# Performance work log

Measured on AMD Instinct MI355X. Metric: run time of the kernel, lower is better.

Reference implementation:

```python
import jax, jax.numpy as jnp
import numpy as np

L, D, H, DH, DF = 4, 512, 8, 64, 2048
B, S = 4, 2048
EPS = 1e-6  # fast-transformers causal-linear eps


def _ln(x, g, b, eps=1e-5):
    mu = jnp.mean(x, axis=-1, keepdims=True)
    var = jnp.var(x, axis=-1, keepdims=True)
    return (x - mu) * jax.lax.rsqrt(var + eps) * g + b


def _causal_linear(Q, K, V):
    # Q, K, V: [B, S, H, DH]; O(N) linear-attention recurrence over S
    Qs = jnp.moveaxis(Q, 1, 0)
    Ks = jnp.moveaxis(K, 1, 0)
    Vs = jnp.moveaxis(V, 1, 0)
    b = Q.shape[0]
    kv0 = jnp.zeros((b, H, DH, DH), Q.dtype)  # running sum of k v^T
    z0 = jnp.zeros((b, H, DH), Q.dtype)       # running sum of k

    def step(carry, qkv):
        kv, z = carry
        q, k, v = qkv  # each [B, H, DH]
        kv = kv + k[..., :, None] * v[..., None, :]
        z = z + k
        num = jnp.einsum('bhd,bhdm->bhm', q, kv)
        den = jnp.einsum('bhd,bhd->bh', q, z) + EPS
        return (kv, z), num / den[..., None]

    _, out = jax.lax.scan(step, (kv0, z0), (Qs, Ks, Vs))
    return jnp.moveaxis(out, 0, 1)  # [B, S, H, DH]


def _layer(x, p):
    Wq, bq, Wk, bk, Wv, bv, Wo, bo, W1, b1, W2, b2, g1, be1, g2, be2 = p
    b, s, _ = x.shape
    q = (x @ Wq + bq).reshape(b, s, H, DH)
    k = (x @ Wk + bk).reshape(b, s, H, DH)
    v = (x @ Wv + bv).reshape(b, s, H, DH)
    Qf = jax.nn.elu(q) + 1.0  # feature map phi(x) = elu(x) + 1
    Kf = jax.nn.elu(k) + 1.0
    a = _causal_linear(Qf, Kf, v).reshape(b, s, D)
    x = x + (a @ Wo + bo)            # residual (dropout=0)
    x = _ln(x, g1, be1)              # post-norm
    y = jax.nn.gelu(x @ W1 + b1, approximate=False) @ W2 + b2
    return _ln(x + y, g2, be2)


def _encoder(h, params, gf, bef):
    def body(x, p):
        return _layer(x, p), None
    x, _ = jax.lax.scan(body, h, params)
    return _ln(x, gf, bef)  # final LayerNorm from builder


def setup_inputs() -> dict:
    key = jax.random.key(0)
    ks = jax.random.split(key, 8)

    def w(k, shape, fan_in):
        return jax.random.normal(k, shape, jnp.float32) * (fan_in ** -0.5)

    return {
        'h': jax.random.normal(ks[0], (B, S, D), jnp.float32),
        'Wq': w(ks[1], (L, D, D), D), 'bq': jnp.zeros((L, D), jnp.float32),
        'Wk': w(ks[2], (L, D, D), D), 'bk': jnp.zeros((L, D), jnp.float32),
        'Wv': w(ks[3], (L, D, D), D), 'bv': jnp.zeros((L, D), jnp.float32),
        'Wo': w(ks[4], (L, D, D), D), 'bo': jnp.zeros((L, D), jnp.float32),
        'W1': w(ks[5], (L, D, DF), D), 'b1': jnp.zeros((L, DF), jnp.float32),
        'W2': w(ks[6], (L, DF, D), DF), 'b2': jnp.zeros((L, D), jnp.float32),
        'g1': jnp.ones((L, D), jnp.float32), 'be1': jnp.zeros((L, D), jnp.float32),
        'g2': jnp.ones((L, D), jnp.float32), 'be2': jnp.zeros((L, D), jnp.float32),
        'gf': jnp.ones((D,), jnp.float32), 'bef': jnp.zeros((D,), jnp.float32),
    }


def reference(h, Wq, bq, Wk, bk, Wv, bv, Wo, bo, W1, b1, W2, b2,
              g1, be1, g2, be2, gf, bef):
    params = (Wq, bq, Wk, bk, Wv, bv, Wo, bo, W1, b1, W2, b2, g1, be1, g2, be2)
    return _encoder(h, params, gf, bef)
```

## Files before the change

kernel.cpp:

```cpp
#include <hip/hip_runtime.h>
#include <hip/hip_bf16.h>
#include <math.h>

#define LAYERS 4
#define DMODEL 512
#define NH 8
#define DH 64
#define DFF 2048
#define NB 4
#define S_LEN 2048
#define MROWS 8192
#define CHUNK 64
#define NCHUNK 32
#define ATT_EPS 1e-6f
#define LN_EPS 1e-5f
#define SEGSTRIDE (MROWS * DMODEL)

typedef __attribute__((ext_vector_type(8))) short short8v;
typedef __attribute__((ext_vector_type(4))) float f32x4;

__device__ __forceinline__ float b2f(unsigned short u) {
    union { float f; unsigned u; } c; c.u = ((unsigned)u) << 16; return c.f;
}
__device__ __forceinline__ unsigned short f2b(float f) {
    union { float f; unsigned u; } c; c.f = f;
    unsigned r = c.u + 0x7FFFu + ((c.u >> 16) & 1u);
    return (unsigned short)(r >> 16);
}
__device__ __forceinline__ void gload16(const void* g, void* l) {
    __builtin_amdgcn_global_load_lds(
        (const __attribute__((address_space(1))) void*)g,
        (__attribute__((address_space(3))) void*)l, 16, 0, 0);
}
__device__ __forceinline__ float elu1f(float v) {
    return (v > 0.f) ? (v + 1.f) : __expf(v);
}
__device__ __forceinline__ float geluf(float v) {
    float u = 0.7978845608028654f * v * (1.f + 0.044715f * v * v);
    float th = 1.f - 2.f / (1.f + __expf(2.f * u));
    return 0.5f * v * (1.f + th);
}

template <int ACT, bool RESID, bool ATOMIC, bool WU, bool WBF16, int KSPLIT>
__global__ __launch_bounds__(512, 4) void gemm8(
    const unsigned short* __restrict__ A,
    const unsigned short* __restrict__ WT,
    const float* __restrict__ b0, const float* __restrict__ b1,
    const float* __restrict__ b2,
    const unsigned short* __restrict__ Xres,
    float* __restrict__ U, unsigned short* __restrict__ Cbf,
    int M, int N, int K)
{
    __shared__ short S[2][16384];

    const int t = threadIdx.x;
    const int m0 = blockIdx.x * 128, n0 = blockIdx.y * 128;
    const int kz = (KSPLIT > 1) ? blockIdx.z : 0;
    const int Kc = K / KSPLIT;
    const int kbeg = kz * Kc;
    const int lane = t & 63, wid = t >> 6;
    const int wm = (wid >> 2) * 64;
    const int wn = (wid & 3) * 32;
    const int fr = lane & 15, kg = lane >> 4;

    const unsigned short* gsrc[4];
    int ldso[4];
#pragma unroll
    for (int r = 0; r < 4; ++r) {
        const int u = (r & 1) ? (t + 512) : t;
        const bool isA = (r < 2);
        const int row = u >> 3, sp = u & 7, sl = sp ^ (row & 7);
        gsrc[r] = (isA ? A + (size_t)(m0 + row) * K
                       : WT + (size_t)(n0 + row) * K) + kbeg + sl * 8;
        ldso[r] = (isA ? 0 : 8192) + u * 8;
    }

    int aoff[2][4], boff[2][2];
#pragma unroll
    for (int h = 0; h < 2; ++h) {
#pragma unroll
        for (int m = 0; m < 4; ++m) {
            const int R = wm + m * 16 + fr;
            aoff[h][m] = R * 64 + (((h * 4 + kg) ^ (R & 7)) * 8);
        }
#pragma unroll
        for (int n = 0; n < 2; ++n) {
            const int R = wn + n * 16 + fr;
            boff[h][n] = 8192 + R * 64 + (((h * 4 + kg) ^ (R & 7)) * 8);
        }
    }

    f32x4 acc[4][2];
#pragma unroll
    for (int m = 0; m < 4; ++m)
#pragma unroll
        for (int n = 0; n < 2; ++n) acc[m][n] = (f32x4){0.f, 0.f, 0.f, 0.f};

#define STAGE(b, kt) do { _Pragma("unroll")                                  \
    for (int r = 0; r < 4; ++r)                                              \
        gload16(gsrc[r] + (size_t)(kt) * 64, &S[b][ldso[r]]); } while (0)

    const int NT = Kc >> 6;
    STAGE(0, 0);

    for (int td = 0; td < NT; ++td) {
        const int b = td & 1;
        if (td + 1 < NT) {
            STAGE(b ^ 1, td + 1);
            __builtin_amdgcn_sched_barrier(0);
            asm volatile("s_waitcnt vmcnt(4)");
        } else {
            __builtin_amdgcn_sched_barrier(0);
            asm volatile("s_waitcnt vmcnt(0)");
        }
        __builtin_amdgcn_sched_barrier(0);
        __builtin_amdgcn_s_barrier();
        __builtin_amdgcn_sched_barrier(0);

        short8v a0[4], b0f[2], a1[4], b1f[2];
#pragma unroll
        for (int m = 0; m < 4; ++m) a0[m] = *(const short8v*)&S[b][aoff[0][m]];
#pragma unroll
        for (int n = 0; n < 2; ++n) b0f[n] = *(const short8v*)&S[b][boff[0][n]];
#pragma unroll
        for (int m = 0; m < 4; ++m) a1[m] = *(const short8v*)&S[b][aoff[1][m]];
#pragma unroll
        for (int n = 0; n < 2; ++n) b1f[n] = *(const short8v*)&S[b][boff[1][n]];

        asm volatile("s_waitcnt lgkmcnt(6)");
        __builtin_amdgcn_sched_barrier(0);
        __builtin_amdgcn_s_setprio(1);
#pragma unroll
        for (int m = 0; m < 4; ++m)
#pragma unroll
            for (int n = 0; n < 2; ++n)
                acc[m][n] = __builtin_amdgcn_mfma_f32_16x16x32_bf16(
                    a0[m], b0f[n], acc[m][n], 0, 0, 0);
        __builtin_amdgcn_s_setprio(0);

        asm volatile("s_waitcnt lgkmcnt(0)");
        __builtin_amdgcn_sched_barrier(0);
        __builtin_amdgcn_s_setprio(1);
#pragma unroll
        for (int m = 0; m < 4; ++m)
#pragma unroll
            for (int n = 0; n < 2; ++n)
                acc[m][n] = __builtin_amdgcn_mfma_f32_16x16x32_bf16(
                    a1[m], b1f[n], acc[m][n], 0, 0, 0);
        __builtin_amdgcn_s_setprio(0);

        __builtin_amdgcn_sched_barrier(0);
        __builtin_amdgcn_s_barrier();
    }
#undef STAGE

    const int seg = (ACT == 3) ? (n0 >> 9) : 0;
    const float* bias = (ACT == 3) ? (seg == 0 ? b0 : (seg == 1 ? b1 : b2)) : b0;
    float bv[2];
#pragma unroll
    for (int n = 0; n < 2; ++n) {
        const int col = n0 + wn + n * 16 + fr;
        bv[n] = bias[(ACT == 3) ? (col - seg * 512) : col];
    }
    if (KSPLIT > 1 && kz != 0) { bv[0] = 0.f; bv[1] = 0.f; }

#pragma unroll
    for (int m = 0; m < 4; ++m)
#pragma unroll
        for (int n = 0; n < 2; ++n)
#pragma unroll
            for (int j = 0; j < 4; ++j) {
                const int row = m0 + wm + m * 16 + (lane >> 4) * 4 + j;
                const int col = n0 + wn + n * 16 + fr;
                float v = acc[m][n][j] + bv[n];
                if (RESID && kz == 0)
                    v += b2f(Xres[(size_t)row * 512 + col]);
                if (ACT == 1) v = elu1f(v);
                else if (ACT == 2) v = geluf(v);
                else if (ACT == 3) { if (seg < 2) v = elu1f(v); }
                if (ATOMIC) {
                    atomicAdd(&U[(size_t)row * N + col], v);
                } else if (WU) {
                    U[(size_t)row * N + col] = v;
                }
                if (WBF16) {
                    if (ACT == 3)
                        Cbf[(size_t)seg * SEGSTRIDE + (size_t)row * 512 + (col - seg * 512)] = f2b(v);
                    else
                        Cbf[(size_t)row * N + col] = f2b(v);
                }
            }
}

__global__ __launch_bounds__(256) void transpose_to_bf16(
    const float* __restrict__ W, unsigned short* __restrict__ WT, int K, int N)
{
    __shared__ float tile[32][33];
    const int k0 = blockIdx.x * 32, n0 = blockIdx.y * 32;
    const int tx = threadIdx.x & 31, ty = threadIdx.x >> 5;
#pragma unroll
    for (int i = ty; i < 32; i += 8)
        tile[i][tx] = W[(size_t)(k0 + i) * N + n0 + tx];
    __syncthreads();
#pragma unroll
    for (int i = ty; i < 32; i += 8)
        WT[(size_t)(n0 + i) * K + k0 + tx] = f2b(tile[tx][i]);
}

__global__ __launch_bounds__(256) void cvt_in(
    const float* __restrict__ h, unsigned short* __restrict__ xb, int n)
{
    const int i = (blockIdx.x * 256 + threadIdx.x) * 8;
    if (i >= n) return;
    f32x4 a = *(const f32x4*)(h + i);
    f32x4 b = *(const f32x4*)(h + i + 4);
    short8v p;
    p[0] = f2b(a[0]); p[1] = f2b(a[1]); p[2] = f2b(a[2]); p[3] = f2b(a[3]);
    p[4] = f2b(b[0]); p[5] = f2b(b[1]); p[6] = f2b(b[2]); p[7] = f2b(b[3]);
    *(short8v*)(xb + i) = p;
}

__device__ __forceinline__ int swzo(int row, int sl) {
    return row * 64 + ((sl ^ (row & 7)) << 3);
}

__global__ __launch_bounds__(256) void attn_stage1(
    const unsigned short* __restrict__ Kf, const unsigned short* __restrict__ Vf,
    unsigned short* __restrict__ KVp, float* __restrict__ zp)
{
    const int c = blockIdx.x, hh = blockIdx.y, bb = blockIdx.z;
    const int t = threadIdx.x;
    const int lane = t & 63, w = t >> 6;
    const int fr = lane & 15, g = lane >> 4;

    __shared__ unsigned short KTs[64 * 72];
    __shared__ unsigned short VTs[64 * 72];

    const size_t rowbase = (size_t)(bb * S_LEN + c * CHUNK);
    const int colbase = hh * DH;

    {
        const int r = lane, cs = w * 16;
        const unsigned short* kp = Kf + (rowbase + r) * DMODEL + colbase + cs;
        const unsigned short* vp = Vf + (rowbase + r) * DMODEL + colbase + cs;
        short8v k0 = *(const short8v*)kp, k1 = *(const short8v*)(kp + 8);
        short8v v0 = *(const short8v*)vp, v1 = *(const short8v*)(vp + 8);
#pragma unroll
        for (int i = 0; i < 8; ++i) {
            KTs[(cs + i) * 72 + r]     = (unsigned short)k0[i];
            KTs[(cs + 8 + i) * 72 + r] = (unsigned short)k1[i];
            VTs[(cs + i) * 72 + r]     = (unsigned short)v0[i];
            VTs[(cs + 8 + i) * 72 + r] = (unsigned short)v1[i];
        }
    }
    __syncthreads();

    f32x4 cacc[4];
#pragma unroll
    for (int nf = 0; nf < 4; ++nf) cacc[nf] = (f32x4){0.f, 0.f, 0.f, 0.f};

    const short8v a0 = *(const short8v*)&VTs[(w * 16 + fr) * 72 + g * 8];
    const short8v a1 = *(const short8v*)&VTs[(w * 16 + fr) * 72 + (4 + g) * 8];
#pragma unroll
    for (int nf = 0; nf < 4; ++nf) {
        short8v bq0 = *(const short8v*)&KTs[(nf * 16 + fr) * 72 + g * 8];
        short8v bq1 = *(const short8v*)&KTs[(nf * 16 + fr) * 72 + (4 + g) * 8];
        cacc[nf] = __builtin_amdgcn_mfma_f32_16x16x32_bf16(a0, bq0, cacc[nf], 0, 0, 0);
        cacc[nf] = __builtin_amdgcn_mfma_f32_16x16x32_bf16(a1, bq1, cacc[nf], 0, 0, 0);
    }

    const size_t base = ((size_t)(bb * NH + hh) * NCHUNK + c) * (DH * DH);
#pragma unroll
    for (int nf = 0; nf < 4; ++nf)
#pragma unroll
        for (int reg = 0; reg < 4; ++reg) {
            const int e = w * 16 + g * 4 + reg;
            const int d = nf * 16 + fr;
            KVp[base + e * 64 + d] = f2b(cacc[nf][reg]);
        }

    if (t < 64) {
        float s = 0.f;
#pragma unroll
        for (int sl = 0; sl < 8; ++sl) {
            short8v kv = *(const short8v*)&KTs[t * 72 + sl * 8];
#pragma unroll
            for (int i = 0; i < 8; ++i) s += b2f((unsigned short)kv[i]);
        }
        zp[((size_t)(bb * NH + hh) * NCHUNK + c) * DH + t] = s;
    }
}

__global__ __launch_bounds__(256) void attn_stage2(
    const unsigned short* __restrict__ KVp, unsigned short* __restrict__ KVb,
    float* __restrict__ zp)
{
    const int bh = blockIdx.x;
    const int e = blockIdx.y * 256 + threadIdx.x;
    const size_t base = (size_t)bh * NCHUNK * (DH * DH) + e;
    float run = 0.f;
#pragma unroll 4
    for (int c = 0; c < NCHUNK; ++c) {
        const float tmp = b2f(KVp[base + (size_t)c * (DH * DH)]);
        KVb[base + (size_t)c * (DH * DH)] = f2b(run);
        run += tmp;
    }
    if (blockIdx.y == 0 && threadIdx.x < DH) {
        float rz = 0.f;
        const size_t zb = (size_t)bh * NCHUNK * DH + threadIdx.x;
#pragma unroll 4
        for (int c = 0; c < NCHUNK; ++c) {
            const float tmp = zp[zb + c * DH];
            zp[zb + c * DH] = rz;
            rz += tmp;
        }
    }
}

__global__ __launch_bounds__(256) void attn_stage3(
    const unsigned short* __restrict__ Qf, const unsigned short* __restrict__ Kf,
    const unsigned short* __restrict__ Vf, const unsigned short* __restrict__ KVb,
    const float* __restrict__ zp, unsigned short* __restrict__ Af)
{
    const int c = blockIdx.x, hh = blockIdx.y, bb = blockIdx.z;
    const int t = threadIdx.x;
    const int lane = t & 63, w = t >> 6;
    const int fr = lane & 15, g = lane >> 4;

    __shared__ unsigned short Qs[4096];
    __shared__ unsigned short Ks[4096];
    __shared__ unsigned short KVts[4096];
    __shared__ unsigned short VTs[64 * 72];
    __shared__ unsigned short Ps[64 * 72];
    __shared__ float zsh[DH];
    __shared__ float den_lds[64];

    const size_t rowbase = (size_t)(bb * S_LEN + c * CHUNK);
    const int colbase = hh * DH;
    const size_t kvbase = ((size_t)(bb * NH + hh) * NCHUNK + c) * (DH * DH);

#pragma unroll
    for (int iss = 0; iss < 2; ++iss) {
        const int u = iss * 256 + t, row = u >> 3, sl = u & 7;
        const int ssl = (sl ^ (row & 7)) * 8;
        gload16(Qf + (rowbase + row) * DMODEL + colbase + ssl, &Qs[(size_t)u * 8]);
        gload16(Kf + (rowbase + row) * DMODEL + colbase + ssl, &Ks[(size_t)u * 8]);
        gload16(KVb + kvbase + row * 64 + ssl, &KVts[(size_t)u * 8]);
    }
    {
        const int r = lane, cs = w * 16;
        const unsigned short* vp = Vf + (rowbase + r) * DMODEL + colbase + cs;
        short8v v0 = *(const short8v*)vp, v1 = *(const short8v*)(vp + 8);
#pragma unroll
        for (int i = 0; i < 8; ++i) {
            VTs[(cs + i) * 72 + r]     = (unsigned short)v0[i];
            VTs[(cs + 8 + i) * 72 + r] = (unsigned short)v1[i];
        }
    }
    if (t < DH) zsh[t] = zp[((size_t)(bb * NH + hh) * NCHUNK + c) * DH + t];
    __syncthreads();

    f32x4 c1[4];
#pragma unroll
    for (int mf = 0; mf < 4; ++mf) c1[mf] = (f32x4){0.f, 0.f, 0.f, 0.f};
    {
        const short8v bq0 = *(const short8v*)&Qs[swzo(w * 16 + fr, g)];
        const short8v bq1 = *(const short8v*)&Qs[swzo(w * 16 + fr, 4 + g)];
#pragma unroll
        for (int mf = 0; mf < 4; ++mf) {
            short8v ak0 = *(const short8v*)&Ks[swzo(mf * 16 + fr, g)];
            short8v ak1 = *(const short8v*)&Ks[swzo(mf * 16 + fr, 4 + g)];
            c1[mf] = __builtin_amdgcn_mfma_f32_16x16x32_bf16(ak0, bq0, c1[mf], 0, 0, 0);
            c1[mf] = __builtin_amdgcn_mfma_f32_16x16x32_bf16(ak1, bq1, c1[mf], 0, 0, 0);
        }
    }

    const int i_my = w * 16 + fr;
    float dint = 0.f;
#pragma unroll
    for (int mf = 0; mf < 4; ++mf)
#pragma unroll
        for (int reg = 0; reg < 4; ++reg) {
            const int j = mf * 16 + g * 4 + reg;
            const float v = (j <= i_my) ? c1[mf][reg] : 0.f;
            dint += v;
            Ps[i_my * 72 + j] = f2b(v);
        }
    dint += __shfl_xor(dint, 16);
    dint += __shfl_xor(dint, 32);

    float dpre = 0.f;
#pragma unroll
    for (int sl = 0; sl < 8; ++sl) {
        short8v qv = *(const short8v*)&Qs[swzo(i_my, sl)];
#pragma unroll
        for (int e = 0; e < 8; ++e) dpre += b2f((unsigned short)qv[e]) * zsh[sl * 8 + e];
    }
    if (g == 0) den_lds[i_my] = dpre + dint + ATT_EPS;

    f32x4 acc[4];
#pragma unroll
    for (int nf = 0; nf < 4; ++nf) acc[nf] = (f32x4){0.f, 0.f, 0.f, 0.f};
    {
        const short8v aq0 = *(const short8v*)&Qs[swzo(w * 16 + fr, g)];
        const short8v aq1 = *(const short8v*)&Qs[swzo(w * 16 + fr, 4 + g)];
#pragma unroll
        for (int nf = 0; nf < 4; ++nf) {
            short8v bkv0 = *(const short8v*)&KVts[swzo(nf * 16 + fr, g)];
            short8v bkv1 = *(const short8v*)&KVts[swzo(nf * 16 + fr, 4 + g)];
            acc[nf] = __builtin_amdgcn_mfma_f32_16x16x32_bf16(aq0, bkv0, acc[nf], 0, 0, 0);
            acc[nf] = __builtin_amdgcn_mfma_f32_16x16x32_bf16(aq1, bkv1, acc[nf], 0, 0, 0);
        }
        const short8v ap0 = *(const short8v*)&Ps[(w * 16 + fr) * 72 + g * 8];
        const short8v ap1 = *(const short8v*)&Ps[(w * 16 + fr) * 72 + (4 + g) * 8];
#pragma unroll
        for (int nf = 0; nf < 4; ++nf) {
            short8v bv0 = *(const short8v*)&VTs[(nf * 16 + fr) * 72 + g * 8];
            short8v bv1 = *(const short8v*)&VTs[(nf * 16 + fr) * 72 + (4 + g) * 8];
            acc[nf] = __builtin_amdgcn_mfma_f32_16x16x32_bf16(ap0, bv0, acc[nf], 0, 0, 0);
            acc[nf] = __builtin_amdgcn_mfma_f32_16x16x32_bf16(ap1, bv1, acc[nf], 0, 0, 0);
        }
    }

#pragma unroll
    for (int reg = 0; reg < 4; ++reg) {
        const int i = w * 16 + g * 4 + reg;
        const float inv = 1.f / den_lds[i];
        unsigned short* dst = Af + (rowbase + i) * DMODEL + colbase;
#pragma unroll
        for (int nf = 0; nf < 4; ++nf)
            dst[nf * 16 + fr] = f2b(acc[nf][reg] * inv);
    }
}

__global__ __launch_bounds__(256) void ln_u2x(float* __restrict__ U,
                                              const float* __restrict__ g,
                                              const float* __restrict__ b,
                                              unsigned short* __restrict__ Xb,
                                              int ZERO)
{
    const size_t row = blockIdx.x * 4 + (threadIdx.x >> 6);
    const int t = threadIdx.x & 63;
    float* ur = U + row * DMODEL;
    f32x4 x0 = *(const f32x4*)&ur[t * 4];
    f32x4 x1 = *(const f32x4*)&ur[256 + t * 4];

    float s  = x0[0] + x0[1] + x0[2] + x0[3] + x1[0] + x1[1] + x1[2] + x1[3];
    float sq = x0[0]*x0[0] + x0[1]*x0[1] + x0[2]*x0[2] + x0[3]*x0[3] +
               x1[0]*x1[0] + x1[1]*x1[1] + x1[2]*x1[2] + x1[3]*x1[3];
#pragma unroll
    for (int m = 1; m < 64; m <<= 1) {
        s  += __shfl_xor(s, m);
        sq += __shfl_xor(sq, m);
    }
    const float mu  = s * (1.f / DMODEL);
    const float var = sq * (1.f / DMODEL) - mu * mu;
    const float rr  = rsqrtf(var + LN_EPS);

    const int c0 = t * 4, c1 = 256 + t * 4;
    f32x4 g0 = *(const f32x4*)&g[c0], g1v = *(const f32x4*)&g[c1];
    f32x4 b0 = *(const f32x4*)&b[c0], b1v = *(const f32x4*)&b[c1];
    unsigned short* xb = Xb + row * DMODEL;
    ushort4 u0, u1;
    u0.x = f2b((x0[0] - mu) * rr * g0[0] + b0[0]);
    u0.y = f2b((x0[1] - mu) * rr * g0[1] + b0[1]);
    u0.z = f2b((x0[2] - mu) * rr * g0[2] + b0[2]);
    u0.w = f2b((x0[3] - mu) * rr * g0[3] + b0[3]);
    u1.x = f2b((x1[0] - mu) * rr * g1v[0] + b1v[0]);
    u1.y = f2b((x1[1] - mu) * rr * g1v[1] + b1v[1]);
    u1.z = f2b((x1[2] - mu) * rr * g1v[2] + b1v[2]);
    u1.w = f2b((x1[3] - mu) * rr * g1v[3] + b1v[3]);
    *(ushort4*)&xb[c0] = u0;
    *(ushort4*)&xb[c1] = u1;
    if (ZERO) {
        *(f32x4*)&ur[c0] = (f32x4){0.f, 0.f, 0.f, 0.f};
        *(f32x4*)&ur[c1] = (f32x4){0.f, 0.f, 0.f, 0.f};
    }
}

__global__ __launch_bounds__(256) void ln_final(const unsigned short* __restrict__ Xb,
                                                const float* __restrict__ g,
                                                const float* __restrict__ b,
                                                float* __restrict__ Out)
{
    const size_t row = blockIdx.x * 4 + (threadIdx.x >> 6);
    const int t = threadIdx.x & 63;
    const unsigned short* xr = Xb + row * DMODEL;
    short8v xv = *(const short8v*)&xr[t * 8];
    float x[8];
#pragma unroll
    for (int i = 0; i < 8; ++i) x[i] = b2f((unsigned short)xv[i]);

    float s = 0.f, sq = 0.f;
#pragma unroll
    for (int i = 0; i < 8; ++i) { s += x[i]; sq += x[i] * x[i]; }
#pragma unroll
    for (int m = 1; m < 64; m <<= 1) {
        s  += __shfl_xor(s, m);
        sq += __shfl_xor(sq, m);
    }
    const float mu  = s * (1.f / DMODEL);
    const float var = sq * (1.f / DMODEL) - mu * mu;
    const float rr  = rsqrtf(var + LN_EPS);

    float* orow = Out + row * DMODEL + t * 8;
    f32x4 o0, o1;
#pragma unroll
    for (int i = 0; i < 4; ++i) {
        o0[i] = (x[i] - mu) * rr * g[t * 8 + i] + b[t * 8 + i];
        o1[i] = (x[4 + i] - mu) * rr * g[t * 8 + 4 + i] + b[t * 8 + 4 + i];
    }
    *(f32x4*)orow = o0;
    *(f32x4*)(orow + 4) = o1;
}

extern "C" void kernel_launch(void* const* d_in, const int* in_sizes, int n_in,
                              void* d_out, int out_size, void* d_ws, size_t ws_size,
                              hipStream_t stream)
{
    const float* h   = (const float*)d_in[0];
    const float* Wq  = (const float*)d_in[1];
    const float* bq  = (const float*)d_in[2];
    const float* Wk  = (const float*)d_in[3];
    const float* bk  = (const float*)d_in[4];
    const float* Wv  = (const float*)d_in[5];
    const float* bv  = (const float*)d_in[6];
    const float* Wo  = (const float*)d_in[7];
    const float* bo  = (const float*)d_in[8];
    const float* W1  = (const float*)d_in[9];
    const float* b1  = (const float*)d_in[10];
    const float* W2  = (const float*)d_in[11];
    const float* b2  = (const float*)d_in[12];
    const float* g1  = (const float*)d_in[13];
    const float* be1 = (const float*)d_in[14];
    const float* g2  = (const float*)d_in[15];
    const float* be2 = (const float*)d_in[16];
    const float* gf  = (const float*)d_in[17];
    const float* bef = (const float*)d_in[18];

    char* ws = (char*)d_ws;
    const size_t MB = 1024 * 1024;
    unsigned short* x_bf = (unsigned short*)(ws);
    unsigned short* qkv  = (unsigned short*)(ws + 8 * MB);
    unsigned short* qb   = qkv;
    unsigned short* kb   = qkv + SEGSTRIDE;
    unsigned short* vb   = qkv + 2 * (size_t)SEGSTRIDE;
    unsigned short* ab   = (unsigned short*)(ws + 32 * MB);
    unsigned short* hid  = (unsigned short*)(ws + 8 * MB);
    unsigned short* KVp  = (unsigned short*)(ws + 40 * MB);
    unsigned short* KVb  = (unsigned short*)(ws + 48 * MB);
    float* U             = (float*)(ws + 40 * MB);
    float* zp            = (float*)(ws + 56 * MB);
    unsigned short* WTall = (unsigned short*)(ws + 57 * MB);

    const int M = MROWS, D = DMODEL, DF = DFF;
    const size_t LSTR = 3 * 1024 * 1024;

    cvt_in<<<dim3(M * D / (256 * 8)), 256, 0, stream>>>(h, x_bf, M * D);
    for (int l = 0; l < LAYERS; ++l) {
        unsigned short* WL = WTall + (size_t)l * LSTR;
        transpose_to_bf16<<<dim3(D / 32, D / 32), 256, 0, stream>>>(Wq + (size_t)l * D * D, WL, D, D);
        transpose_to_bf16<<<dim3(D / 32, D / 32), 256, 0, stream>>>(Wk + (size_t)l * D * D, WL + 262144, D, D);
        transpose_to_bf16<<<dim3(D / 32, D / 32), 256, 0, stream>>>(Wv + (size_t)l * D * D, WL + 524288, D, D);
        transpose_to_bf16<<<dim3(D / 32, D / 32), 256, 0, stream>>>(Wo + (size_t)l * D * D, WL + 786432, D, D);
        transpose_to_bf16<<<dim3(D / 32, DF / 32), 256, 0, stream>>>(W1 + (size_t)l * D * DF, WL + 1048576, D, DF);
        transpose_to_bf16<<<dim3(DF / 32, D / 32), 256, 0, stream>>>(W2 + (size_t)l * DF * D, WL + 2097152, DF, D);
    }

    for (int l = 0; l < LAYERS; ++l) {
        unsigned short* WL = WTall + (size_t)l * LSTR;
        const unsigned short* WqkvT = WL;
        const unsigned short* WoT   = WL + 786432;
        const unsigned short* W1T   = WL + 1048576;
        const unsigned short* W2T   = WL + 2097152;

        gemm8<3, false, false, false, true, 1>
            <<<dim3(M / 128, 1536 / 128), 512, 0, stream>>>(
            x_bf, WqkvT, bq + (size_t)l * D, bk + (size_t)l * D, bv + (size_t)l * D,
            nullptr, nullptr, qkv, M, 1536, D);

        attn_stage1<<<dim3(NCHUNK, NH, NB), 256, 0, stream>>>(kb, vb, KVp, zp);
        attn_stage2<<<dim3(NB * NH, 16), 256, 0, stream>>>(KVp, KVb, zp);
        attn_stage3<<<dim3(NCHUNK, NH, NB), 256, 0, stream>>>(qb, kb, vb, KVb, zp, ab);

        gemm8<0, true, false, true, false, 1>
            <<<dim3(M / 128, D / 128), 512, 0, stream>>>(
            ab, WoT, bo + (size_t)l * D, nullptr, nullptr, x_bf, U, nullptr, M, D, D);
        ln_u2x<<<dim3(M / 4), 256, 0, stream>>>(U, g1 + (size_t)l * D, be1 + (size_t)l * D, x_bf, 1);

        gemm8<2, false, false, false, true, 1>
            <<<dim3(M / 128, DF / 128), 512, 0, stream>>>(
            x_bf, W1T, b1 + (size_t)l * DF, nullptr, nullptr, nullptr, nullptr, hid, M, DF, D);
        gemm8<0, true, true, false, false, 2>
            <<<dim3(M / 128, D / 128, 2), 512, 0, stream>>>(
            hid, W2T, b2 + (size_t)l * D, nullptr, nullptr, x_bf, U, nullptr, M, D, DF);
        ln_u2x<<<dim3(M / 4), 256, 0, stream>>>(U, g2 + (size_t)l * D, be2 + (size_t)l * D, x_bf, 0);
    }

    ln_final<<<dim3(M / 4), 256, 0, stream>>>(x_bf, gf, bef, (float*)d_out);
}
```

Baseline: 637.3 us.

## Rework GEMM into triple-buffered BK=32 kernel with wider tiles and non-atomic split-K

The GEMM kernel moves from a double-buffered BK=64 pipeline to a triple-buffered BK=32 pipeline that prefetches two stages ahead. This drops one barrier per iteration, and the N tile becomes a template parameter so the QKV and FFN1 GEMMs can use 256-wide tiles. Split-K for W2 now writes two bf16 partials instead of fp32 atomics, and a new LayerNorm kernel sums the partials, which removes the atomic traffic and the zeroing pass. The weight transposes are batched across layers with a z grid dimension. In exchange there is more register and LDS pressure per block, and the split-K partials are rounded to bf16 before the sum.

```diff
diff --git a/kernel.cpp b/kernel.cpp
--- a/kernel.cpp
+++ b/kernel.cpp
@@ -41,8 +41,8 @@
     return 0.5f * v * (1.f + th);
 }
 
-template <int ACT, bool RESID, bool ATOMIC, bool WU, bool WBF16, int KSPLIT>
-__global__ __launch_bounds__(512, 4) void gemm8(
+template <int BN, int ACT, bool RESID, bool WU, bool WBF16, int KSPLIT>
+__global__ __launch_bounds__(512, 4) void gemm3b(
     const unsigned short* __restrict__ A,
     const unsigned short* __restrict__ WT,
     const float* __restrict__ b0, const float* __restrict__ b1,
@@ -51,92 +51,84 @@
     float* __restrict__ U, unsigned short* __restrict__ Cbf,
     int M, int N, int K)
 {
-    __shared__ short S[2][16384];
+    constexpr int NREP = BN / 64;
+    constexpr int NLD  = 1 + BN / 128;
+    constexpr int TSH  = (128 + BN) * 32;
+    __shared__ short S[3][TSH];
 
     const int t = threadIdx.x;
-    const int m0 = blockIdx.x * 128, n0 = blockIdx.y * 128;
+    const int m0 = blockIdx.x * 128, n0 = blockIdx.y * BN;
     const int kz = (KSPLIT > 1) ? blockIdx.z : 0;
     const int Kc = K / KSPLIT;
     const int kbeg = kz * Kc;
     const int lane = t & 63, wid = t >> 6;
     const int wm = (wid >> 2) * 64;
-    const int wn = (wid & 3) * 32;
+    const int wn = (wid & 3) * (BN / 4);
     const int fr = lane & 15, kg = lane >> 4;
 
-    const unsigned short* gsrc[4];
-    int ldso[4];
-#pragma unroll
-    for (int r = 0; r < 4; ++r) {
-        const int u = (r & 1) ? (t + 512) : t;
-        const bool isA = (r < 2);
-        const int row = u >> 3, sp = u & 7, sl = sp ^ (row & 7);
-        gsrc[r] = (isA ? A + (size_t)(m0 + row) * K
-                       : WT + (size_t)(n0 + row) * K) + kbeg + sl * 8;
-        ldso[r] = (isA ? 0 : 8192) + u * 8;
-    }
-
-    int aoff[2][4], boff[2][2];
-#pragma unroll
-    for (int h = 0; h < 2; ++h) {
-#pragma unroll
-        for (int m = 0; m < 4; ++m) {
-            const int R = wm + m * 16 + fr;
-            aoff[h][m] = R * 64 + (((h * 4 + kg) ^ (R & 7)) * 8);
-        }
-#pragma unroll
-        for (int n = 0; n < 2; ++n) {
-            const int R = wn + n * 16 + fr;
-            boff[h][n] = 8192 + R * 64 + (((h * 4 + kg) ^ (R & 7)) * 8);
-        }
-    }
-
-    f32x4 acc[4][2];
+    const unsigned short* gsrc[NLD];
+    int ldso[NLD];
+    {
+        const int rowA = t >> 2, spA = t & 3;
+        gsrc[0] = A + (size_t)(m0 + rowA) * K + kbeg + (spA ^ ((rowA >> 1) & 3)) * 8;
+        ldso[0] = t * 8;
+#pragma unroll
+        for (int r = 1; r < NLD; ++r) {
+            const int u = (r - 1) * 512 + t;
+            const int row = u >> 2, sp = u & 3;
+            gsrc[r] = WT + (size_t)(n0 + row) * K + kbeg + (sp ^ ((row >> 1) & 3)) * 8;
+            ldso[r] = 4096 + u * 8;
+        }
+    }
+
+    int aoff[4], boff[NREP];
+#pragma unroll
+    for (int m = 0; m < 4; ++m) {
+        const int R = wm + m * 16 + fr;
+        aoff[m] = R * 32 + ((kg ^ ((R >> 1) & 3)) << 3);
+    }
+#pragma unroll
+    for (int n = 0; n < NREP; ++n) {
+        const int R = wn + n * 16 + fr;
+        boff[n] = 4096 + R * 32 + ((kg ^ ((R >> 1) & 3)) << 3);
+    }
+
+    f32x4 acc[4][NREP];
 #pragma unroll
     for (int m = 0; m < 4; ++m)
 #pragma unroll
-        for (int n = 0; n < 2; ++n) acc[m][n] = (f32x4){0.f, 0.f, 0.f, 0.f};
+        for (int n = 0; n < NREP; ++n) acc[m][n] = (f32x4){0.f, 0.f, 0.f, 0.f};
 
 #define STAGE(b, kt) do { _Pragma("unroll")                                  \
-    for (int r = 0; r < 4; ++r)                                              \
-        gload16(gsrc[r] + (size_t)(kt) * 64, &S[b][ldso[r]]); } while (0)
-
-    const int NT = Kc >> 6;
+    for (int r = 0; r < NLD; ++r)                                            \
+        gload16(gsrc[r] + (size_t)(kt) * 32, &S[b][ldso[r]]); } while (0)
+
+    const int NT = Kc >> 5;
     STAGE(0, 0);
-
+    STAGE(1, 1);
+
+    int b = 0;
     for (int td = 0; td < NT; ++td) {
-        const int b = td & 1;
         if (td + 1 < NT) {
-            STAGE(b ^ 1, td + 1);
-            __builtin_amdgcn_sched_barrier(0);
-            asm volatile("s_waitcnt vmcnt(4)");
+            if (NLD == 3) asm volatile("s_waitcnt vmcnt(3)");
+            else          asm volatile("s_waitcnt vmcnt(2)");
         } else {
-            __builtin_amdgcn_sched_barrier(0);
             asm volatile("s_waitcnt vmcnt(0)");
         }
         __builtin_amdgcn_sched_barrier(0);
         __builtin_amdgcn_s_barrier();
         __builtin_amdgcn_sched_barrier(0);
 
-        short8v a0[4], b0f[2], a1[4], b1f[2];
-#pragma unroll
-        for (int m = 0; m < 4; ++m) a0[m] = *(const short8v*)&S[b][aoff[0][m]];
-#pragma unroll
-        for (int n = 0; n < 2; ++n) b0f[n] = *(const short8v*)&S[b][boff[0][n]];
-#pragma unroll
-        for (int m = 0; m < 4; ++m) a1[m] = *(const short8v*)&S[b][aoff[1][m]];
-#pragma unroll
-        for (int n = 0; n < 2; ++n) b1f[n] = *(const short8v*)&S[b][boff[1][n]];
-
-        asm volatile("s_waitcnt lgkmcnt(6)");
-        __builtin_amdgcn_sched_barrier(0);
-        __builtin_amdgcn_s_setprio(1);
-#pragma unroll
-        for (int m = 0; m < 4; ++m)
-#pragma unroll
-            for (int n = 0; n < 2; ++n)
-                acc[m][n] = __builtin_amdgcn_mfma_f32_16x16x32_bf16(
-                    a0[m], b0f[n], acc[m][n], 0, 0, 0);
-        __builtin_amdgcn_s_setprio(0);
+        if (td + 2 < NT) {
+            const int nb = (b + 2 >= 3) ? (b - 1) : (b + 2);
+            STAGE(nb, td + 2);
+        }
+
+        short8v af[4], bf[NREP];
+#pragma unroll
+        for (int m = 0; m < 4; ++m) af[m] = *(const short8v*)&S[b][aoff[m]];
+#pragma unroll
+        for (int n = 0; n < NREP; ++n) bf[n] = *(const short8v*)&S[b][boff[n]];
 
         asm volatile("s_waitcnt lgkmcnt(0)");
         __builtin_amdgcn_sched_barrier(0);
@@ -144,30 +136,33 @@
 #pragma unroll
         for (int m = 0; m < 4; ++m)
 #pragma unroll
-            for (int n = 0; n < 2; ++n)
+            for (int n = 0; n < NREP; ++n)
                 acc[m][n] = __builtin_amdgcn_mfma_f32_16x16x32_bf16(
-                    a1[m], b1f[n], acc[m][n], 0, 0, 0);
+                    af[m], bf[n], acc[m][n], 0, 0, 0);
         __builtin_amdgcn_s_setprio(0);
-
         __builtin_amdgcn_sched_barrier(0);
-        __builtin_amdgcn_s_barrier();
+
+        b = (b + 1 >= 3) ? 0 : (b + 1);
     }
 #undef STAGE
 
     const int seg = (ACT == 3) ? (n0 >> 9) : 0;
     const float* bias = (ACT == 3) ? (seg == 0 ? b0 : (seg == 1 ? b1 : b2)) : b0;
-    float bv[2];
-#pragma unroll
-    for (int n = 0; n < 2; ++n) {
+    float bv[NREP];
+#pragma unroll
+    for (int n = 0; n < NREP; ++n) {
         const int col = n0 + wn + n * 16 + fr;
         bv[n] = bias[(ACT == 3) ? (col - seg * 512) : col];
     }
-    if (KSPLIT > 1 && kz != 0) { bv[0] = 0.f; bv[1] = 0.f; }
+    if (KSPLIT > 1 && kz != 0) {
+#pragma unroll
+        for (int n = 0; n < NREP; ++n) bv[n] = 0.f;
+    }
 
 #pragma unroll
     for (int m = 0; m < 4; ++m)
 #pragma unroll
-        for (int n = 0; n < 2; ++n)
+        for (int n = 0; n < NREP; ++n)
 #pragma unroll
             for (int j = 0; j < 4; ++j) {
                 const int row = m0 + wm + m * 16 + (lane >> 4) * 4 + j;
@@ -175,17 +170,15 @@
                 float v = acc[m][n][j] + bv[n];
                 if (RESID && kz == 0)
                     v += b2f(Xres[(size_t)row * 512 + col]);
-                if (ACT == 1) v = elu1f(v);
-                else if (ACT == 2) v = geluf(v);
+                if (ACT == 2) v = geluf(v);
                 else if (ACT == 3) { if (seg < 2) v = elu1f(v); }
-                if (ATOMIC) {
-                    atomicAdd(&U[(size_t)row * N + col], v);
-                } else if (WU) {
+                if (WU)
                     U[(size_t)row * N + col] = v;
-                }
                 if (WBF16) {
                     if (ACT == 3)
                         Cbf[(size_t)seg * SEGSTRIDE + (size_t)row * 512 + (col - seg * 512)] = f2b(v);
+                    else if (KSPLIT > 1)
+                        Cbf[(size_t)kz * SEGSTRIDE + (size_t)row * N + col] = f2b(v);
                     else
                         Cbf[(size_t)row * N + col] = f2b(v);
                 }
@@ -193,9 +186,13 @@
 }
 
 __global__ __launch_bounds__(256) void transpose_to_bf16(
-    const float* __restrict__ W, unsigned short* __restrict__ WT, int K, int N)
+    const float* __restrict__ W, unsigned short* __restrict__ WT, int K, int N,
+    size_t wstride, size_t tstride)
 {
     __shared__ float tile[32][33];
+    const int l = blockIdx.z;
+    W += (size_t)l * wstride;
+    WT += (size_t)l * tstride;
     const int k0 = blockIdx.x * 32, n0 = blockIdx.y * 32;
     const int tx = threadIdx.x & 31, ty = threadIdx.x >> 5;
 #pragma unroll
@@ -433,15 +430,14 @@
     }
 }
 
-__global__ __launch_bounds__(256) void ln_u2x(float* __restrict__ U,
+__global__ __launch_bounds__(256) void ln_u2x(const float* __restrict__ U,
                                               const float* __restrict__ g,
                                               const float* __restrict__ b,
-                                              unsigned short* __restrict__ Xb,
-                                              int ZERO)
+                                              unsigned short* __restrict__ Xb)
 {
     const size_t row = blockIdx.x * 4 + (threadIdx.x >> 6);
     const int t = threadIdx.x & 63;
-    float* ur = U + row * DMODEL;
+    const float* ur = U + row * DMODEL;
     f32x4 x0 = *(const f32x4*)&ur[t * 4];
     f32x4 x1 = *(const f32x4*)&ur[256 + t * 4];
 
@@ -472,10 +468,41 @@
     u1.w = f2b((x1[3] - mu) * rr * g1v[3] + b1v[3]);
     *(ushort4*)&xb[c0] = u0;
     *(ushort4*)&xb[c1] = u1;
-    if (ZERO) {
-        *(f32x4*)&ur[c0] = (f32x4){0.f, 0.f, 0.f, 0.f};
-        *(f32x4*)&ur[c1] = (f32x4){0.f, 0.f, 0.f, 0.f};
-    }
+}
+
+__global__ __launch_bounds__(256) void ln_2b(const unsigned short* __restrict__ U0b,
+                                             const unsigned short* __restrict__ U1b,
+                                             const float* __restrict__ g,
+                                             const float* __restrict__ b,
+                                             unsigned short* __restrict__ Xb)
+{
+    const size_t row = blockIdx.x * 4 + (threadIdx.x >> 6);
+    const int t = threadIdx.x & 63;
+    short8v v0 = *(const short8v*)&U0b[row * DMODEL + t * 8];
+    short8v v1 = *(const short8v*)&U1b[row * DMODEL + t * 8];
+    float x[8];
+#pragma unroll
+    for (int i = 0; i < 8; ++i)
+        x[i] = b2f((unsigned short)v0[i]) + b2f((unsigned short)v1[i]);
+
+    float s = 0.f, sq = 0.f;
+#pragma unroll
+    for (int i = 0; i < 8; ++i) { s += x[i]; sq += x[i] * x[i]; }
+#pragma unroll
+    for (int m = 1; m < 64; m <<= 1) {
+        s  += __shfl_xor(s, m);
+        sq += __shfl_xor(sq, m);
+    }
+    const float mu  = s * (1.f / DMODEL);
+    const float var = sq * (1.f / DMODEL) - mu * mu;
+    const float rr  = rsqrtf(var + LN_EPS);
+
+    unsigned short* xb = Xb + row * DMODEL + t * 8;
+    short8v p;
+#pragma unroll
+    for (int i = 0; i < 8; ++i)
+        p[i] = f2b((x[i] - mu) * rr * g[t * 8 + i] + b[t * 8 + i]);
+    *(short8v*)xb = p;
 }
 
 __global__ __launch_bounds__(256) void ln_final(const unsigned short* __restrict__ Xb,
@@ -550,6 +577,7 @@
     unsigned short* KVp  = (unsigned short*)(ws + 40 * MB);
     unsigned short* KVb  = (unsigned short*)(ws + 48 * MB);
     float* U             = (float*)(ws + 40 * MB);
+    unsigned short* U01b = (unsigned short*)(ws + 40 * MB);
     float* zp            = (float*)(ws + 56 * MB);
     unsigned short* WTall = (unsigned short*)(ws + 57 * MB);
 
@@ -557,15 +585,18 @@
     const size_t LSTR = 3 * 1024 * 1024;
 
     cvt_in<<<dim3(M * D / (256 * 8)), 256, 0, stream>>>(h, x_bf, M * D);
-    for (int l = 0; l < LAYERS; ++l) {
-        unsigned short* WL = WTall + (size_t)l * LSTR;
-        transpose_to_bf16<<<dim3(D / 32, D / 32), 256, 0, stream>>>(Wq + (size_t)l * D * D, WL, D, D);
-        transpose_to_bf16<<<dim3(D / 32, D / 32), 256, 0, stream>>>(Wk + (size_t)l * D * D, WL + 262144, D, D);
-        transpose_to_bf16<<<dim3(D / 32, D / 32), 256, 0, stream>>>(Wv + (size_t)l * D * D, WL + 524288, D, D);
-        transpose_to_bf16<<<dim3(D / 32, D / 32), 256, 0, stream>>>(Wo + (size_t)l * D * D, WL + 786432, D, D);
-        transpose_to_bf16<<<dim3(D / 32, DF / 32), 256, 0, stream>>>(W1 + (size_t)l * D * DF, WL + 1048576, D, DF);
-        transpose_to_bf16<<<dim3(DF / 32, D / 32), 256, 0, stream>>>(W2 + (size_t)l * DF * D, WL + 2097152, DF, D);
-    }
+    transpose_to_bf16<<<dim3(D / 32, D / 32, LAYERS), 256, 0, stream>>>(
+        Wq, WTall, D, D, (size_t)D * D, LSTR);
+    transpose_to_bf16<<<dim3(D / 32, D / 32, LAYERS), 256, 0, stream>>>(
+        Wk, WTall + 262144, D, D, (size_t)D * D, LSTR);
+    transpose_to_bf16<<<dim3(D / 32, D / 32, LAYERS), 256, 0, stream>>>(
+        Wv, WTall + 524288, D, D, (size_t)D * D, LSTR);
+    transpose_to_bf16<<<dim3(D / 32, D / 32, LAYERS), 256, 0, stream>>>(
+        Wo, WTall + 786432, D, D, (size_t)D * D, LSTR);
+    transpose_to_bf16<<<dim3(D / 32, DF / 32, LAYERS), 256, 0, stream>>>(
+        W1, WTall + 1048576, D, DF, (size_t)D * DF, LSTR);
+    transpose_to_bf16<<<dim3(DF / 32, D / 32, LAYERS), 256, 0, stream>>>(
+        W2, WTall + 2097152, DF, D, (size_t)DF * D, LSTR);
 
     for (int l = 0; l < LAYERS; ++l) {
         unsigned short* WL = WTall + (size_t)l * LSTR;
@@ -574,8 +605,8 @@
         const unsigned short* W1T   = WL + 1048576;
         const unsigned short* W2T   = WL + 2097152;
 
-        gemm8<3, false, false, false, true, 1>
-            <<<dim3(M / 128, 1536 / 128), 512, 0, stream>>>(
+        gemm3b<256, 3, false, false, true, 1>
+            <<<dim3(M / 128, 1536 / 256), 512, 0, stream>>>(
             x_bf, WqkvT, bq + (size_t)l * D, bk + (size_t)l * D, bv + (size_t)l * D,
             nullptr, nullptr, qkv, M, 1536, D);
 
@@ -583,18 +614,20 @@
         attn_stage2<<<dim3(NB * NH, 16), 256, 0, stream>>>(KVp, KVb, zp);
         attn_stage3<<<dim3(NCHUNK, NH, NB), 256, 0, stream>>>(qb, kb, vb, KVb, zp, ab);
 
-        gemm8<0, true, false, true, false, 1>
+        gemm3b<128, 0, true, true, false, 1>
             <<<dim3(M / 128, D / 128), 512, 0, stream>>>(
             ab, WoT, bo + (size_t)l * D, nullptr, nullptr, x_bf, U, nullptr, M, D, D);
-        ln_u2x<<<dim3(M / 4), 256, 0, stream>>>(U, g1 + (size_t)l * D, be1 + (size_t)l * D, x_bf, 1);
-
-        gemm8<2, false, false, false, true, 1>
-            <<<dim3(M / 128, DF / 128), 512, 0, stream>>>(
-            x_bf, W1T, b1 + (size_t)l * DF, nullptr, nullptr, nullptr, nullptr, hid, M, DF, D);
-        gemm8<0, true, true, false, false, 2>
+        ln_u2x<<<dim3(M / 4), 256, 0, stream>>>(U, g1 + (size_t)l * D, be1 + (size_t)l * D, x_bf);
+
+        gemm3b<256, 2, false, false, true, 1>
+            <<<dim3(M / 128, DF / 256), 512, 0, stream>>>(
+            x_bf, W1T, b1 + (size_t)l * DF, nullptr, nullptr,
+            nullptr, nullptr, hid, M, DF, D);
+        gemm3b<128, 0, true, false, true, 2>
             <<<dim3(M / 128, D / 128, 2), 512, 0, stream>>>(
-            hid, W2T, b2 + (size_t)l * D, nullptr, nullptr, x_bf, U, nullptr, M, D, DF);
-        ln_u2x<<<dim3(M / 4), 256, 0, stream>>>(U, g2 + (size_t)l * D, be2 + (size_t)l * D, x_bf, 0);
+            hid, W2T, b2 + (size_t)l * D, nullptr, nullptr, x_bf, nullptr, U01b, M, D, DF);
+        ln_2b<<<dim3(M / 4), 256, 0, stream>>>(U01b, U01b + SEGSTRIDE,
+            g2 + (size_t)l * D, be2 + (size_t)l * D, x_bf);
     }
 
     ln_final<<<dim3(M / 4), 256, 0, stream>>>(x_bf, gf, bef, (float*)d_out);
```

Result: faster. 552.8 us (-13.3%).
